# Kernel tuning notes

Hardware: AMD Instinct MI355X
Metric: run time of the kernel (lower is better)

## Reference

```python
import jax, jax.numpy as jnp
import numpy as np

N_NODES = 40000
N_EDGES = 640000
EMB = 128
OUT_EMB = 256
NUM_DENSE = 3
NUM_TARGETS = 12
NUM_RADIAL = 6


def setup_inputs() -> dict:
    key = jax.random.key(0)
    ks = jax.random.split(key, 8)
    n_atoms = jax.random.normal(ks[0], (N_NODES, EMB), dtype=jnp.float32)
    x = jax.random.normal(ks[1], (N_EDGES, EMB), dtype=jnp.float32)
    rbf = jax.random.normal(ks[2], (N_EDGES, NUM_RADIAL), dtype=jnp.float32)
    idnb_i = jax.random.randint(ks[3], (N_EDGES,), 0, N_NODES, dtype=jnp.int64 if jax.config.read('jax_enable_x64') else jnp.int32)
    s = 0.05
    W_rbf = jax.random.normal(ks[4], (NUM_RADIAL, EMB), dtype=jnp.float32) * s
    W_up = jax.random.normal(ks[5], (EMB, OUT_EMB), dtype=jnp.float32) * s
    W_mlp = jax.random.normal(ks[6], (NUM_DENSE, OUT_EMB, OUT_EMB), dtype=jnp.float32) * s
    b_mlp = jnp.zeros((NUM_DENSE, OUT_EMB), dtype=jnp.float32)
    W_final = jax.random.normal(ks[7], (OUT_EMB, NUM_TARGETS), dtype=jnp.float32) * s
    return {"n_atoms": n_atoms, "x": x, "rbf": rbf, "idnb_i": idnb_i,
            "W_rbf": W_rbf, "W_up": W_up, "W_mlp": W_mlp, "b_mlp": b_mlp,
            "W_final": W_final}


def reference(n_atoms, x, rbf, idnb_i, W_rbf, W_up, W_mlp, b_mlp, W_final):
    # g = Dense(emb_size, no bias)(rbf): [M, EMB]
    g = rbf @ W_rbf
    # elementwise edge gate
    xe = g * x                                  # [M, EMB]
    # scatter-sum edges -> nodes (pooling_method='sum')
    pooled = jax.ops.segment_sum(xe, idnb_i, num_segments=n_atoms.shape[0])  # [N, EMB]
    # up-projection, no bias
    h = pooled @ W_up                           # [N, OUT_EMB]
    # GraphMLP: num_dense layers, swish activation, with bias
    for i in range(W_mlp.shape[0]):
        h = jax.nn.silu(h @ W_mlp[i] + b_mlp[i])
    # final output projection, no bias
    return h @ W_final                          # [N, NUM_TARGETS]
```

## Files before the change

### kernel.cpp

```cpp
#include <hip/hip_runtime.h>
#include <hip/hip_fp16.h>
#include <math.h>

constexpr int kNodes   = 40000;
constexpr int kEdges   = 640000;
constexpr int kEmb     = 128;
constexpr int kOut     = 256;
constexpr int kTargets = 12;
constexpr int kRadial  = 6;

typedef float        f32x4 __attribute__((ext_vector_type(4)));
typedef unsigned int u32x4 __attribute__((ext_vector_type(4)));

typedef __attribute__((address_space(1))) const void gvoid;
typedef __attribute__((address_space(3))) void       lvoid;

__device__ __forceinline__ unsigned short f2h(float f) {
  return __half_as_ushort(__float2half(f));
}
__device__ __forceinline__ void mfma_f16(f32x4& c, u32x4 a, u32x4 b) {
  asm volatile("v_mfma_f32_16x16x32_f16 %0, %1, %2, %0" : "+v"(c) : "v"(a), "v"(b));
}

__global__ __launch_bounds__(256) void prep_weights(
    const float* __restrict__ Wup, const float* __restrict__ Wmlp,
    const float* __restrict__ Wfin,
    unsigned short* __restrict__ WtUp, unsigned short* __restrict__ WtM,
    unsigned short* __restrict__ WtFin, int* __restrict__ counts) {
  const int id = blockIdx.x * 256 + threadIdx.x;
  if (id < kNodes) counts[id] = 0;

  if (id < 32768) {
    const int e = id & 7, u = id >> 3;
    const int l = u & 63, j = (u >> 6) & 3, wv = (u >> 8) & 3, c = u >> 10;
    const int n = wv * 64 + j * 16 + (l & 15);
    const int k = c * 32 + (l >> 4) * 8 + e;
    WtUp[id] = f2h(Wup[k * 256 + n]);
    return;
  }
  const int id2 = id - 32768;
  if (id2 < 3 * 65536) {
    const int L = id2 >> 16, r = id2 & 65535;
    const int e = r & 7, u = r >> 3;
    const int l = u & 63, j = (u >> 6) & 3, wv = (u >> 8) & 3, c = u >> 10;
    const int n = wv * 64 + j * 16 + (l & 15);
    const int k = c * 32 + (l >> 4) * 8 + e;
    WtM[id2] = f2h(Wmlp[L * 65536 + k * 256 + n]);
    return;
  }
  const int id3 = id2 - 3 * 65536;
  if (id3 < 16 * 256) {
    const int n = id3 >> 8, k = id3 & 255;
    WtFin[id3] = (n < kTargets) ? f2h(Wfin[k * kTargets + n]) : (unsigned short)0;
  }
}

__global__ __launch_bounds__(256) void hist_kernel(const int* __restrict__ idnb,
                                                   int* __restrict__ counts) {
  const int e = blockIdx.x * 256 + threadIdx.x;
  if (e < kEdges) atomicAdd(&counts[idnb[e]], 1);
}

__global__ __launch_bounds__(256) void scan_pass1(const int* __restrict__ counts,
                                                  int* __restrict__ bsum) {
  __shared__ int sm[256];
  const int idx = blockIdx.x * 256 + threadIdx.x;
  sm[threadIdx.x] = (idx < kNodes) ? counts[idx] : 0;
  __syncthreads();
  for (int d = 128; d > 0; d >>= 1) {
    if (threadIdx.x < d) sm[threadIdx.x] += sm[threadIdx.x + d];
    __syncthreads();
  }
  if (threadIdx.x == 0) bsum[blockIdx.x] = sm[0];
}

__global__ __launch_bounds__(256) void scan_pass3(const int* __restrict__ counts,
                                                  const int* __restrict__ bsum,
                                                  int* __restrict__ offs,
                                                  int* __restrict__ next,
                                                  int nblk) {
  __shared__ int sm[256];
  __shared__ int base;
  const int t = threadIdx.x;
  sm[t] = (t < nblk && t < (int)blockIdx.x) ? bsum[t] : 0;
  __syncthreads();
  for (int d = 128; d > 0; d >>= 1) {
    if (t < d) sm[t] += sm[t + d];
    __syncthreads();
  }
  if (t == 0) base = sm[0];
  __syncthreads();

  const int idx = blockIdx.x * 256 + t;
  const int v = (idx < kNodes) ? counts[idx] : 0;
  sm[t] = v;
  __syncthreads();
  for (int d = 1; d < 256; d <<= 1) {
    const int xsh = (t >= d) ? sm[t - d] : 0;
    __syncthreads();
    sm[t] += xsh;
    __syncthreads();
  }
  if (idx < kNodes) {
    const int e = base + sm[t] - v;
    offs[idx] = e;
    next[idx] = e;
  }
  if (blockIdx.x == 0 && t == 0) offs[kNodes] = kEdges;
}

__global__ __launch_bounds__(256) void fill_kernel(const int* __restrict__ idnb,
                                                   int* __restrict__ next,
                                                   int* __restrict__ edgeIdx) {
  const int e = blockIdx.x * 256 + threadIdx.x;
  if (e < kEdges) {
    const int p = atomicAdd(&next[idnb[e]], 1);
    edgeIdx[p] = e;
  }
}

__global__ __launch_bounds__(256) void gather_kernel(
    const float* __restrict__ x, const float* __restrict__ rbf,
    const int* __restrict__ offs, const int* __restrict__ edgeIdx,
    const float* __restrict__ W_rbf, unsigned short* __restrict__ pooled) {
  __shared__ float wLds[kRadial * kEmb];
  for (int i = threadIdx.x; i < kRadial * kEmb; i += 256) wLds[i] = W_rbf[i];
  __syncthreads();

  const int sub = threadIdx.x & 31;
  const int n   = blockIdx.x * 8 + (threadIdx.x >> 5);

  f32x4 w[kRadial];
#pragma unroll
  for (int j = 0; j < kRadial; ++j)
    w[j] = *(const f32x4*)(wLds + j * kEmb + sub * 4);

  const int beg = offs[n], end = offs[n + 1];
  f32x4 acc0 = {0.f, 0.f, 0.f, 0.f};
  f32x4 acc1 = {0.f, 0.f, 0.f, 0.f};

  int i = beg;
  for (; i + 1 < end; i += 2) {
    const int e0 = edgeIdx[i];
    const int e1 = edgeIdx[i + 1];
    const float2 a0 = *(const float2*)(rbf + (size_t)e0 * kRadial);
    const float2 b0 = *(const float2*)(rbf + (size_t)e0 * kRadial + 2);
    const float2 c0 = *(const float2*)(rbf + (size_t)e0 * kRadial + 4);
    const float2 a1 = *(const float2*)(rbf + (size_t)e1 * kRadial);
    const float2 b1 = *(const float2*)(rbf + (size_t)e1 * kRadial + 2);
    const float2 c1 = *(const float2*)(rbf + (size_t)e1 * kRadial + 4);
    const f32x4 xv0 = __builtin_nontemporal_load(
        (const f32x4*)(x + (size_t)e0 * kEmb + sub * 4));
    const f32x4 xv1 = __builtin_nontemporal_load(
        (const f32x4*)(x + (size_t)e1 * kEmb + sub * 4));
    const f32x4 g0 = a0.x * w[0] + a0.y * w[1] + b0.x * w[2] +
                     b0.y * w[3] + c0.x * w[4] + c0.y * w[5];
    const f32x4 g1 = a1.x * w[0] + a1.y * w[1] + b1.x * w[2] +
                     b1.y * w[3] + c1.x * w[4] + c1.y * w[5];
    acc0 += g0 * xv0;
    acc1 += g1 * xv1;
  }
  if (i < end) {
    const int e0 = edgeIdx[i];
    const float2 a0 = *(const float2*)(rbf + (size_t)e0 * kRadial);
    const float2 b0 = *(const float2*)(rbf + (size_t)e0 * kRadial + 2);
    const float2 c0 = *(const float2*)(rbf + (size_t)e0 * kRadial + 4);
    const f32x4 xv0 = __builtin_nontemporal_load(
        (const f32x4*)(x + (size_t)e0 * kEmb + sub * 4));
    const f32x4 g0 = a0.x * w[0] + a0.y * w[1] + b0.x * w[2] +
                     b0.y * w[3] + c0.x * w[4] + c0.y * w[5];
    acc0 += g0 * xv0;
  }
  const f32x4 acc = acc0 + acc1;

  ushort4 hv;
  hv.x = f2h(acc.x);
  hv.y = f2h(acc.y);
  hv.z = f2h(acc.z);
  hv.w = f2h(acc.w);
  *(ushort4*)(pooled + (size_t)n * kEmb + sub * 4) = hv;
}

__global__ __launch_bounds__(256) void fused_mlp(
    const unsigned short* __restrict__ pooled,
    const unsigned short* __restrict__ WtUp,
    const unsigned short* __restrict__ WtM,
    const unsigned short* __restrict__ WtFin,
    const float* __restrict__ b_mlp, float* __restrict__ out) {
  __shared__ unsigned short act[64][266];
  __shared__ unsigned short sB[2][8192];

  const int tid     = threadIdx.x;
  const int rowBase = blockIdx.x * 64;
  const int w    = tid >> 6;
  const int lane = tid & 63;
  const int lrow = lane & 15;
  const int kgrp = lane >> 4;

#pragma unroll
  for (int p = 0; p < 4; ++p) {
    const int q = p * 256 + tid;
    const int r = q >> 4, c = q & 15;
    *(u32x4*)&act[r][c * 8] =
        *(const u32x4*)(pooled + (size_t)(rowBase + r) * kEmb + c * 8);
  }
  __syncthreads();

  for (int l = 0; l < 4; ++l) {
    const int nc = (l == 0) ? 4 : 8;
    const unsigned short* W = (l == 0) ? WtUp : WtM + (size_t)(l - 1) * 65536;

    float bj[4] = {0.f, 0.f, 0.f, 0.f};
    if (l >= 1) {
      const float* bias = b_mlp + (size_t)(l - 1) * kOut;
#pragma unroll
      for (int j = 0; j < 4; ++j) bj[j] = bias[w * 64 + j * 16 + lrow];
      asm volatile("" ::"v"(bj[0]), "v"(bj[1]), "v"(bj[2]), "v"(bj[3]));
    }

#pragma unroll
    for (int j = 0; j < 4; ++j)
      __builtin_amdgcn_global_load_lds(
          (gvoid*)(W + w * 2048 + j * 512 + lane * 8),
          (lvoid*)&sB[0][w * 2048 + j * 512], 16, 0, 0);

    f32x4 acc[4][4];
#pragma unroll
    for (int i = 0; i < 4; ++i)
#pragma unroll
      for (int j = 0; j < 4; ++j) acc[i][j] = f32x4{0.f, 0.f, 0.f, 0.f};

    int buf = 0;
    for (int c = 0; c < nc; ++c) {
      if (c + 1 < nc) {
        const unsigned short* Wn = W + (size_t)(c + 1) * 8192;
#pragma unroll
        for (int j = 0; j < 4; ++j)
          __builtin_amdgcn_global_load_lds(
              (gvoid*)(Wn + w * 2048 + j * 512 + lane * 8),
              (lvoid*)&sB[buf ^ 1][w * 2048 + j * 512], 16, 0, 0);
        asm volatile("s_waitcnt vmcnt(4)" ::: "memory");
      } else {
        asm volatile("s_waitcnt vmcnt(0)" ::: "memory");
      }
      u32x4 a[4], b[4];
#pragma unroll
      for (int i = 0; i < 4; ++i)
        a[i] = *(const u32x4*)&act[i * 16 + lrow][c * 32 + kgrp * 8];
#pragma unroll
      for (int j = 0; j < 4; ++j)
        b[j] = *(const u32x4*)&sB[buf][w * 2048 + j * 512 + lane * 8];
      __builtin_amdgcn_s_setprio(1);
#pragma unroll
      for (int j = 0; j < 4; ++j)
#pragma unroll
        for (int i = 0; i < 4; ++i) mfma_f16(acc[i][j], a[i], b[j]);
      __builtin_amdgcn_s_setprio(0);
      buf ^= 1;
    }

    __syncthreads();
#pragma unroll
    for (int j = 0; j < 4; ++j) {
      const int col = w * 64 + j * 16 + lrow;
#pragma unroll
      for (int i = 0; i < 4; ++i) {
#pragma unroll
        for (int r = 0; r < 4; ++r) {
          float v = acc[i][j][r];
          if (l >= 1) {
            v += bj[j];
            v = v / (1.f + __expf(-v));
          }
          act[i * 16 + kgrp * 4 + r][col] = f2h(v);
        }
      }
    }
    __syncthreads();
  }

  unsigned short (*sWf)[266] = (unsigned short(*)[266]) & sB[0][0];
  float (*sPart)[64][16]     = (float(*)[64][16]) & sB[1][0];
#pragma unroll
  for (int p = 0; p < 2; ++p) {
    const int q = p * 256 + tid;
    const int n = q >> 5, c = q & 31;
    *(u32x4*)&sWf[n][c * 8] = *(const u32x4*)(WtFin + (size_t)n * 256 + c * 8);
  }
  __syncthreads();

  f32x4 accF[4];
#pragma unroll
  for (int i = 0; i < 4; ++i) accF[i] = f32x4{0.f, 0.f, 0.f, 0.f};
#pragma unroll
  for (int s = 0; s < 2; ++s) {
    const int cc = w * 2 + s;
    const u32x4 b = *(const u32x4*)&sWf[lrow][cc * 32 + kgrp * 8];
#pragma unroll
    for (int i = 0; i < 4; ++i) {
      const u32x4 a = *(const u32x4*)&act[i * 16 + lrow][cc * 32 + kgrp * 8];
      mfma_f16(accF[i], a, b);
    }
  }
#pragma unroll
  for (int i = 0; i < 4; ++i)
#pragma unroll
    for (int r = 0; r < 4; ++r)
      sPart[w][i * 16 + kgrp * 4 + r][lrow] = accF[i][r];
  __syncthreads();

  for (int q = tid; q < 64 * kTargets; q += 256) {
    const int r = q / kTargets, t = q % kTargets;
    out[(size_t)(rowBase + r) * kTargets + t] =
        sPart[0][r][t] + sPart[1][r][t] + sPart[2][r][t] + sPart[3][r][t];
  }
}

extern "C" void kernel_launch(void* const* d_in, const int* in_sizes, int n_in,
                              void* d_out, int out_size, void* d_ws, size_t ws_size,
                              hipStream_t stream) {
  const float* x      = (const float*)d_in[1];
  const float* rbf    = (const float*)d_in[2];
  const int*   idnb   = (const int*)d_in[3];
  const float* W_rbf  = (const float*)d_in[4];
  const float* W_up   = (const float*)d_in[5];
  const float* W_mlp  = (const float*)d_in[6];
  const float* b_mlp  = (const float*)d_in[7];
  const float* W_fin  = (const float*)d_in[8];
  float* out = (float*)d_out;

  char* wp = (char*)d_ws;
  auto alloc = [&](size_t bytes) -> void* {
    void* r = wp;
    wp += (bytes + 255) & ~(size_t)255;
    return r;
  };
  unsigned short* pooled = (unsigned short*)alloc((size_t)kNodes * kEmb * 2);
  unsigned short* WtUp   = (unsigned short*)alloc(32768 * 2);
  unsigned short* WtM    = (unsigned short*)alloc(3 * 65536 * 2);
  unsigned short* WtFin  = (unsigned short*)alloc(16 * 256 * 2);
  int* counts  = (int*)alloc((size_t)kNodes * 4);
  int* offs    = (int*)alloc((size_t)(kNodes + 8) * 4);
  int* next    = (int*)alloc((size_t)kNodes * 4);
  int* edgeIdx = (int*)alloc((size_t)kEdges * 4);
  int* bsum    = (int*)alloc(256 * 4);

  constexpr int nScanBlk = (kNodes + 255) / 256;
  constexpr int prepElems = 32768 + 3 * 65536 + 16 * 256;

  prep_weights<<<(prepElems + 255) / 256, 256, 0, stream>>>(
      W_up, W_mlp, W_fin, WtUp, WtM, WtFin, counts);
  hist_kernel<<<kEdges / 256, 256, 0, stream>>>(idnb, counts);
  scan_pass1<<<nScanBlk, 256, 0, stream>>>(counts, bsum);
  scan_pass3<<<nScanBlk, 256, 0, stream>>>(counts, bsum, offs, next, nScanBlk);
  fill_kernel<<<kEdges / 256, 256, 0, stream>>>(idnb, next, edgeIdx);
  gather_kernel<<<kNodes / 8, 256, 0, stream>>>(x, rbf, offs, edgeIdx, W_rbf,
                                                pooled);
  fused_mlp<<<kNodes / 64, 256, 0, stream>>>(pooled, WtUp, WtM, WtFin, b_mlp,
                                             out);
}
```

Before: 222.5 us.

## Merge CSR build kernels into one cooperative kernel with grid syncs

Replaces the histogram, two scan passes and fill kernels (plus the counts zeroing) with one cooperative kernel of 1024 blocks that separates the phases with grid.sync(). The aim is to remove several kernel launch gaps and inter-kernel drains in the CSR construction. Weight prep moves after the gather. Grid-wide barriers have their own cost, and the histogram and fill loops now run grid-stride over fewer threads.

```diff
diff --git a/kernel.cpp b/kernel.cpp
--- a/kernel.cpp
+++ b/kernel.cpp
@@ -1,6 +1,9 @@
 #include <hip/hip_runtime.h>
 #include <hip/hip_fp16.h>
+#include <hip/hip_cooperative_groups.h>
 #include <math.h>
+
+namespace cg = cooperative_groups;
 
 constexpr int kNodes   = 40000;
 constexpr int kEdges   = 640000;
@@ -22,13 +25,78 @@
   asm volatile("v_mfma_f32_16x16x32_f16 %0, %1, %2, %0" : "+v"(c) : "v"(a), "v"(b));
 }
 
+__global__ __launch_bounds__(256) void csr_coop(
+    const int* __restrict__ idnb, int* __restrict__ counts,
+    int* __restrict__ offs, int* __restrict__ next,
+    int* __restrict__ edgeIdx, int* __restrict__ bsum) {
+  cg::grid_group grid = cg::this_grid();
+  __shared__ int sm[256];
+  __shared__ int base;
+
+  const int t    = threadIdx.x;
+  const int gtid = blockIdx.x * 256 + t;
+  const int gsz  = gridDim.x * 256;
+  constexpr int nScanBlk = (kNodes + 255) / 256;
+
+  for (int i = gtid; i < kNodes; i += gsz) counts[i] = 0;
+  grid.sync();
+
+  for (int e = gtid; e < kEdges; e += gsz) atomicAdd(&counts[idnb[e]], 1);
+  grid.sync();
+
+  if (blockIdx.x < nScanBlk) {
+    const int idx = blockIdx.x * 256 + t;
+    sm[t] = (idx < kNodes) ? counts[idx] : 0;
+    __syncthreads();
+    for (int d = 128; d > 0; d >>= 1) {
+      if (t < d) sm[t] += sm[t + d];
+      __syncthreads();
+    }
+    if (t == 0) bsum[blockIdx.x] = sm[0];
+  }
+  grid.sync();
+
+  if (blockIdx.x < nScanBlk) {
+    sm[t] = (t < nScanBlk && t < (int)blockIdx.x) ? bsum[t] : 0;
+    __syncthreads();
+    for (int d = 128; d > 0; d >>= 1) {
+      if (t < d) sm[t] += sm[t + d];
+      __syncthreads();
+    }
+    if (t == 0) base = sm[0];
+    __syncthreads();
+
+    const int idx = blockIdx.x * 256 + t;
+    const int v = (idx < kNodes) ? counts[idx] : 0;
+    sm[t] = v;
+    __syncthreads();
+    for (int d = 1; d < 256; d <<= 1) {
+      const int xsh = (t >= d) ? sm[t - d] : 0;
+      __syncthreads();
+      sm[t] += xsh;
+      __syncthreads();
+    }
+    if (idx < kNodes) {
+      const int e = base + sm[t] - v;
+      offs[idx] = e;
+      next[idx] = e;
+    }
+    if (blockIdx.x == 0 && t == 0) offs[kNodes] = kEdges;
+  }
+  grid.sync();
+
+  for (int e = gtid; e < kEdges; e += gsz) {
+    const int p = atomicAdd(&next[idnb[e]], 1);
+    edgeIdx[p] = e;
+  }
+}
+
 __global__ __launch_bounds__(256) void prep_weights(
     const float* __restrict__ Wup, const float* __restrict__ Wmlp,
     const float* __restrict__ Wfin,
     unsigned short* __restrict__ WtUp, unsigned short* __restrict__ WtM,
-    unsigned short* __restrict__ WtFin, int* __restrict__ counts) {
+    unsigned short* __restrict__ WtFin) {
   const int id = blockIdx.x * 256 + threadIdx.x;
-  if (id < kNodes) counts[id] = 0;
 
   if (id < 32768) {
     const int e = id & 7, u = id >> 3;
@@ -52,70 +120,6 @@
   if (id3 < 16 * 256) {
     const int n = id3 >> 8, k = id3 & 255;
     WtFin[id3] = (n < kTargets) ? f2h(Wfin[k * kTargets + n]) : (unsigned short)0;
-  }
-}
-
-__global__ __launch_bounds__(256) void hist_kernel(const int* __restrict__ idnb,
-                                                   int* __restrict__ counts) {
-  const int e = blockIdx.x * 256 + threadIdx.x;
-  if (e < kEdges) atomicAdd(&counts[idnb[e]], 1);
-}
-
-__global__ __launch_bounds__(256) void scan_pass1(const int* __restrict__ counts,
-                                                  int* __restrict__ bsum) {
-  __shared__ int sm[256];
-  const int idx = blockIdx.x * 256 + threadIdx.x;
-  sm[threadIdx.x] = (idx < kNodes) ? counts[idx] : 0;
-  __syncthreads();
-  for (int d = 128; d > 0; d >>= 1) {
-    if (threadIdx.x < d) sm[threadIdx.x] += sm[threadIdx.x + d];
-    __syncthreads();
-  }
-  if (threadIdx.x == 0) bsum[blockIdx.x] = sm[0];
-}
-
-__global__ __launch_bounds__(256) void scan_pass3(const int* __restrict__ counts,
-                                                  const int* __restrict__ bsum,
-                                                  int* __restrict__ offs,
-                                                  int* __restrict__ next,
-                                                  int nblk) {
-  __shared__ int sm[256];
-  __shared__ int base;
-  const int t = threadIdx.x;
-  sm[t] = (t < nblk && t < (int)blockIdx.x) ? bsum[t] : 0;
-  __syncthreads();
-  for (int d = 128; d > 0; d >>= 1) {
-    if (t < d) sm[t] += sm[t + d];
-    __syncthreads();
-  }
-  if (t == 0) base = sm[0];
-  __syncthreads();
-
-  const int idx = blockIdx.x * 256 + t;
-  const int v = (idx < kNodes) ? counts[idx] : 0;
-  sm[t] = v;
-  __syncthreads();
-  for (int d = 1; d < 256; d <<= 1) {
-    const int xsh = (t >= d) ? sm[t - d] : 0;
-    __syncthreads();
-    sm[t] += xsh;
-    __syncthreads();
-  }
-  if (idx < kNodes) {
-    const int e = base + sm[t] - v;
-    offs[idx] = e;
-    next[idx] = e;
-  }
-  if (blockIdx.x == 0 && t == 0) offs[kNodes] = kEdges;
-}
-
-__global__ __launch_bounds__(256) void fill_kernel(const int* __restrict__ idnb,
-                                                   int* __restrict__ next,
-                                                   int* __restrict__ edgeIdx) {
-  const int e = blockIdx.x * 256 + threadIdx.x;
-  if (e < kEdges) {
-    const int p = atomicAdd(&next[idnb[e]], 1);
-    edgeIdx[p] = e;
   }
 }
 
@@ -345,17 +349,19 @@
   int* edgeIdx = (int*)alloc((size_t)kEdges * 4);
   int* bsum    = (int*)alloc(256 * 4);
 
-  constexpr int nScanBlk = (kNodes + 255) / 256;
   constexpr int prepElems = 32768 + 3 * 65536 + 16 * 256;
 
-  prep_weights<<<(prepElems + 255) / 256, 256, 0, stream>>>(
-      W_up, W_mlp, W_fin, WtUp, WtM, WtFin, counts);
-  hist_kernel<<<kEdges / 256, 256, 0, stream>>>(idnb, counts);
-  scan_pass1<<<nScanBlk, 256, 0, stream>>>(counts, bsum);
-  scan_pass3<<<nScanBlk, 256, 0, stream>>>(counts, bsum, offs, next, nScanBlk);
-  fill_kernel<<<kEdges / 256, 256, 0, stream>>>(idnb, next, edgeIdx);
+  {
+    const int* a0 = idnb;
+    int *a1 = counts, *a2 = offs, *a3 = next, *a4 = edgeIdx, *a5 = bsum;
+    void* args[] = {&a0, &a1, &a2, &a3, &a4, &a5};
+    hipLaunchCooperativeKernel((void*)csr_coop, dim3(1024), dim3(256), args, 0,
+                               stream);
+  }
   gather_kernel<<<kNodes / 8, 256, 0, stream>>>(x, rbf, offs, edgeIdx, W_rbf,
                                                 pooled);
+  prep_weights<<<(prepElems + 255) / 256, 256, 0, stream>>>(
+      W_up, W_mlp, W_fin, WtUp, WtM, WtFin);
   fused_mlp<<<kNodes / 64, 256, 0, stream>>>(pooled, WtUp, WtM, WtFin, b_mlp,
                                              out);
 }
```

After: 587.9 us. 164% more time.
